# Kernel optimization log

Measured on AMD Instinct MI355X. Metric: run time of the kernel, lower is better.

## Reference

```python
import jax, jax.numpy as jnp
import numpy as np

N = 50000      # nodes
E = 250000     # edges
IN = 256       # in_channels
OUT = 256      # out_channels
H = 4          # heads
C = OUT // H   # per-head channels = 64
MSG = 128
TIME = 64
ED = MSG + TIME + 2   # edge_dim = 194


def _glorot(k, shape):
    return (jax.random.normal(k, shape, jnp.float32) / np.sqrt(shape[0])).astype(jnp.float32)


def setup_inputs() -> dict:
    ks = jax.random.split(jax.random.key(0), 16)
    z = lambda: jnp.zeros((H * C,), jnp.float32)
    inp = {
        "x": jax.random.normal(ks[0], (N, IN), jnp.float32),
        "edge_index": jax.random.randint(ks[1], (2, E), 0, N),
        "edge_attr": jax.random.normal(ks[2], (E, ED), jnp.float32),
        # conv1 params (in_channels=IN)
        "Wq1": _glorot(ks[3], (IN, H * C)), "bq1": z(),
        "Wk1": _glorot(ks[4], (IN, H * C)), "bk1": z(),
        "Wv1": _glorot(ks[5], (IN, H * C)), "bv1": z(),
        "We1": _glorot(ks[6], (ED, H * C)),              # lin_edge has no bias in PyG
        "Ws1": _glorot(ks[7], (IN, H * C)), "bs1": z(),  # skip/root connection
        # conv2 params (in_channels=OUT)
        "Wq2": _glorot(ks[8], (OUT, H * C)), "bq2": z(),
        "Wk2": _glorot(ks[9], (OUT, H * C)), "bk2": z(),
        "Wv2": _glorot(ks[10], (OUT, H * C)), "bv2": z(),
        "We2": _glorot(ks[11], (ED, H * C)),
        "Ws2": _glorot(ks[12], (OUT, H * C)), "bs2": z(),
    }
    return inp


def _tconv(x, src, dst, edge_attr, Wq, bq, Wk, bk, Wv, bv, We, Ws, bs):
    """PyG TransformerConv (heads=H, concat=True, root_weight=True), eval mode."""
    n = x.shape[0]
    q = (x @ Wq + bq).reshape(n, H, C)
    k = (x @ Wk + bk).reshape(n, H, C)
    v = (x @ Wv + bv).reshape(n, H, C)
    e = (edge_attr @ We).reshape(-1, H, C)          # [E,H,C]
    kj = k[src] + e                                  # key + edge embedding
    vj = v[src] + e                                  # value + edge embedding
    logits = jnp.einsum('ehc,ehc->eh', q[dst], kj) / np.sqrt(C)  # [E,H]
    # segment softmax over incoming edges of each dst node
    m = jax.lax.stop_gradient(jax.ops.segment_max(logits, dst, num_segments=n))
    ex = jnp.exp(logits - m[dst])
    denom = jax.ops.segment_sum(ex, dst, num_segments=n)
    a = ex / (denom[dst] + 1e-16)                    # [E,H]
    agg = jax.ops.segment_sum(vj * a[:, :, None], dst, num_segments=n)  # [N,H,C]
    return agg.reshape(n, H * C) + x @ Ws + bs


def reference(x, edge_index, edge_attr,
              Wq1, bq1, Wk1, bk1, Wv1, bv1, We1, Ws1, bs1,
              Wq2, bq2, Wk2, bk2, Wv2, bv2, We2, Ws2, bs2):
    src, dst = edge_index[0], edge_index[1]
    h = jax.nn.relu(_tconv(x, src, dst, edge_attr,
                           Wq1, bq1, Wk1, bk1, Wv1, bv1, We1, Ws1, bs1))
    # dropout is identity in eval mode
    return _tconv(h, src, dst, edge_attr,
                  Wq2, bq2, Wk2, bk2, Wv2, bv2, We2, Ws2, bs2)
```

## Files before the change

### kernel.cpp

```cpp
#include <hip/hip_runtime.h>

#define N_NODES 50000
#define N_EDGES 250000
#define DIM 256
#define ED 194
#define EDP 224
#define MP_NODE 50048
#define MP_EDGE 250112

typedef __bf16 bf16x8 __attribute__((ext_vector_type(8)));
typedef float f32x4 __attribute__((ext_vector_type(4)));
typedef short s16x8 __attribute__((ext_vector_type(8)));
typedef short s16x4 __attribute__((ext_vector_type(4)));
typedef unsigned short u16x8 __attribute__((ext_vector_type(8)));

__device__ __forceinline__ float bf2f(unsigned short b){
  union { unsigned int u; float f; } v; v.u = ((unsigned int)b)<<16; return v.f;
}
__device__ __forceinline__ short f2bf(float f){
  union { float f; unsigned int u; } v; v.f = f;
  unsigned int u = v.u;
  return (short)((u + 0x7fffu + ((u>>16)&1u))>>16);
}

__device__ __forceinline__ void gload_lds16(const void* g, void* l){
  __builtin_amdgcn_global_load_lds(
      (const __attribute__((address_space(1))) unsigned int*)g,
      (__attribute__((address_space(3))) unsigned int*)l, 16, 0, 0);
}

__global__ __launch_bounds__(256) void convert_x_kernel(
    const float* __restrict__ x, short* __restrict__ xb, int* __restrict__ deg)
{
  int idx = blockIdx.x*256 + threadIdx.x;
  if (idx < N_NODES) deg[idx] = 0;
  s16x4 o;
  if (idx < N_NODES*64){
    float4 a = *(const float4*)(x + (size_t)idx*4);
    o[0]=f2bf(a.x); o[1]=f2bf(a.y); o[2]=f2bf(a.z); o[3]=f2bf(a.w);
  } else {
    o[0]=0; o[1]=0; o[2]=0; o[3]=0;
  }
  *(s16x4*)(xb + (size_t)idx*4) = o;
}

#define E_ROWS 32
__global__ __launch_bounds__(256) void convert_e_kernel(
    const float* __restrict__ ea, short* __restrict__ eb)
{
  __shared__ float lds[E_ROWS*ED];
  int row0 = blockIdx.x * E_ROWS;
  int tid = threadIdx.x;
  int base = row0 * ED;
  int valid = N_EDGES*ED - base;

  for (int i = tid; i < E_ROWS*ED/4; i += 256){
    float4 v;
    if (i*4 < valid) v = *(const float4*)(ea + base + i*4);
    else             v = make_float4(0.f,0.f,0.f,0.f);
    *(float4*)(lds + i*4) = v;
  }
  __syncthreads();

  for (int u = tid; u < E_ROWS*28; u += 256){
    int row = u / 28;
    int c8  = u - row*28;
    int col = c8*8;
    s16x8 o;
    if (col + 8 <= ED){
      #pragma unroll
      for (int j2=0;j2<4;j2++){
        float2 f = *(const float2*)(lds + row*ED + col + j2*2);
        o[j2*2]   = f2bf(f.x);
        o[j2*2+1] = f2bf(f.y);
      }
    } else {
      #pragma unroll
      for (int j=0;j<8;j++){
        int c = col + j;
        o[j] = (c < ED) ? f2bf(lds[row*ED + c]) : (short)0;
      }
    }
    *(s16x8*)(eb + (size_t)(row0+row)*EDP + col) = o;
  }
}

__global__ __launch_bounds__(256) void prep_weights_all(
    const float* __restrict__ Wq1, const float* __restrict__ Wk1,
    const float* __restrict__ Wv1, const float* __restrict__ Ws1,
    const float* __restrict__ We1,
    const float* __restrict__ bq1, const float* __restrict__ bk1,
    const float* __restrict__ bv1, const float* __restrict__ bs1,
    const float* __restrict__ Wq2, const float* __restrict__ Wk2,
    const float* __restrict__ Wv2, const float* __restrict__ Ws2,
    const float* __restrict__ We2,
    const float* __restrict__ bq2, const float* __restrict__ bk2,
    const float* __restrict__ bv2, const float* __restrict__ bs2,
    short* __restrict__ WtN1, short* __restrict__ WtN2,
    short* __restrict__ WtE, float* __restrict__ biasN1, float* __restrict__ biasN2)
{
  __shared__ short lds[64*65];
  int b = blockIdx.x, tid = threadIdx.x;
  if (b < 128){
    int conv = b>>6, bb = b&63;
    int mat = bb>>4, tile = bb&15;
    int i0 = (tile>>2)*64, o0 = (tile&3)*64;
    const float* W = conv ? ((mat==0)?Wq2:((mat==1)?Wk2:((mat==2)?Wv2:Ws2)))
                          : ((mat==0)?Wq1:((mat==1)?Wk1:((mat==2)?Wv1:Ws1)));
    short* WtN = conv ? WtN2 : WtN1;
    #pragma unroll
    for (int t=0;t<16;t++){
      int idx = t*256+tid; int r = idx>>6, c = idx&63;
      lds[r*65+c] = f2bf(W[(size_t)(i0+r)*256 + o0 + c]);
    }
    __syncthreads();
    #pragma unroll
    for (int t=0;t<4;t++){
      int idx = t*256+tid; int r = idx>>4, c4 = (idx&15)*4;
      s16x4 o;
      o[0]=lds[(c4+0)*65+r]; o[1]=lds[(c4+1)*65+r];
      o[2]=lds[(c4+2)*65+r]; o[3]=lds[(c4+3)*65+r];
      *(s16x4*)(WtN + (mat<<16) + (o0+r)*256 + i0 + c4) = o;
    }
  } else if (b < 160){
    int b2 = b-128;
    int k0 = (b2>>3)*64, o0 = (b2&7)*64;
    const float* We = (o0 < 256) ? We1 : We2;
    int oc = o0 & 255;
    #pragma unroll
    for (int t=0;t<16;t++){
      int idx = t*256+tid; int r = idx>>6, c = idx&63;
      int k = k0+r;
      lds[r*65+c] = (k<ED) ? f2bf(We[(size_t)k*256 + oc + c]) : (short)0;
    }
    __syncthreads();
    #pragma unroll
    for (int t=0;t<4;t++){
      int idx = t*256+tid; int r = idx>>4, c4 = (idx&15)*4;
      if (k0 + c4 < EDP){
        s16x4 o;
        o[0]=lds[(c4+0)*65+r]; o[1]=lds[(c4+1)*65+r];
        o[2]=lds[(c4+2)*65+r]; o[3]=lds[(c4+3)*65+r];
        *(s16x4*)(WtE + (size_t)(o0+r)*EDP + k0 + c4) = o;
      }
    }
  } else {
    int conv = b - 160;
    float* biasN = conv ? biasN2 : biasN1;
    for (int t = tid; t < 1024; t += 256){
      const float* bb = conv ? ((t<256)?bq2:((t<512)?bk2:((t<768)?bv2:bs2)))
                             : ((t<256)?bq1:((t<512)?bk1:((t<768)?bv1:bs1)));
      biasN[t] = bb[t&255];
    }
  }
}

__global__ __launch_bounds__(256) void count_deg(const int* __restrict__ dst, int* __restrict__ deg){
  int e = blockIdx.x*256 + threadIdx.x;
  if (e < N_EDGES) atomicAdd(&deg[dst[e]], 1);
}
#define SCAN_NBLK 196
__global__ __launch_bounds__(256) void scan_p1(const int* __restrict__ deg, int* __restrict__ part){
  int t = threadIdx.x;
  int i = blockIdx.x*256 + t;
  int v = (i<N_NODES)? deg[i] : 0;
  #pragma unroll
  for (int off=32; off; off>>=1) v += __shfl_xor(v, off, 64);
  __shared__ int s[4];
  if ((t&63)==0) s[t>>6] = v;
  __syncthreads();
  if (t==0) part[blockIdx.x] = s[0]+s[1]+s[2]+s[3];
}
__global__ __launch_bounds__(256) void scan_p2(int* __restrict__ part){
  __shared__ int s[256];
  int t = threadIdx.x;
  int v = (t<SCAN_NBLK)? part[t] : 0;
  s[t] = v; __syncthreads();
  for (int off=1; off<256; off<<=1){
    int x = (t>=off)? s[t-off] : 0;
    __syncthreads();
    s[t] += x;
    __syncthreads();
  }
  part[t] = (t==0)? 0 : s[t-1];
}
__global__ __launch_bounds__(256) void scan_p3(const int* __restrict__ deg,
    const int* __restrict__ part, int* __restrict__ rowptr, int* __restrict__ cursor){
  __shared__ int s[256];
  int t = threadIdx.x;
  int i = blockIdx.x*256 + t;
  int v = (i<N_NODES)? deg[i] : 0;
  s[t] = v; __syncthreads();
  for (int off=1; off<256; off<<=1){
    int x = (t>=off)? s[t-off] : 0;
    __syncthreads();
    s[t] += x;
    __syncthreads();
  }
  if (i < N_NODES){ rowptr[i+1] = part[blockIdx.x] + s[t]; cursor[i] = 0; }
  if (i == 0) rowptr[0] = 0;
}
__global__ __launch_bounds__(256) void scatter_edges(
    const int* __restrict__ src, const int* __restrict__ dst,
    const int* __restrict__ rowptr, int* __restrict__ cursor, int2* __restrict__ csr)
{
  int e = blockIdx.x*256 + threadIdx.x;
  if (e < N_EDGES){
    int d = dst[e];
    int pos = atomicAdd(&cursor[d], 1);
    csr[rowptr[d] + pos] = make_int2(src[e]<<11, e<<10);
  }
}

template<int K, int NLD, bool HAS_BIAS, int SWZ_NB>
__global__ __launch_bounds__(256) void gemm_bt(
    const short* __restrict__ A, const short* __restrict__ Bt,
    const float* __restrict__ bias, short* __restrict__ out, int M)
{
  __shared__ short As[128*32];
  __shared__ short Bs[128*32];
  int tid = threadIdx.x;
  int lane = tid & 63, wave = tid >> 6;

  int mblk, nblk;
  if (SWZ_NB > 0){
    int bid = blockIdx.x;
    int MB  = gridDim.x / SWZ_NB;
    int MB8 = MB & ~7;
    int body = MB8 * SWZ_NB;
    if (bid < body){
      int xcd = bid & 7, w = bid >> 3;
      nblk = w % SWZ_NB;
      mblk = (w / SWZ_NB) * 8 + xcd;
    } else {
      int r = bid - body;
      mblk = MB8 + r / SWZ_NB;
      nblk = r % SWZ_NB;
    }
  } else {
    mblk = blockIdx.x; nblk = blockIdx.y;
  }
  int m0 = mblk*128, n0 = nblk*128;

  int srow = tid>>2, scol = (tid&3)*8;
  const short* gA = A + (size_t)(m0+srow)*K + scol;
  const short* gB = Bt + (size_t)(n0+srow)*K + scol;
  short* ldsA1 = As + wave*512;
  short* ldsA2 = As + 2048 + wave*512;
  short* ldsB1 = Bs + wave*512;
  short* ldsB2 = Bs + 2048 + wave*512;

  int wr = wave>>1, wc = wave&1;
  int fr = lane & 15;
  int kq = lane >> 4;
  f32x4 acc[4][4];
  #pragma unroll
  for (int a=0;a<4;a++)
    #pragma unroll
    for (int b=0;b<4;b++) acc[a][b] = (f32x4){0.f,0.f,0.f,0.f};

  for (int k0=0; k0<K; k0+=32){
    __syncthreads();
    gload_lds16(gA + k0,                ldsA1);
    gload_lds16(gA + (size_t)64*K + k0, ldsA2);
    gload_lds16(gB + k0,                ldsB1);
    gload_lds16(gB + (size_t)64*K + k0, ldsB2);
    __syncthreads();

    bf16x8 af[4], bf[4];
    const short* ar = As + (wr*64 + fr)*32 + kq*8;
    const short* br = Bs + (wc*64 + fr)*32 + kq*8;
    #pragma unroll
    for (int fm=0;fm<4;fm++) af[fm] = *(const bf16x8*)(ar + fm*512);
    #pragma unroll
    for (int fn=0;fn<4;fn++) bf[fn] = *(const bf16x8*)(br + fn*512);
    #pragma unroll
    for (int fm=0;fm<4;fm++)
      #pragma unroll
      for (int fn=0;fn<4;fn++)
        acc[fm][fn] = __builtin_amdgcn_mfma_f32_16x16x32_bf16(af[fm], bf[fn], acc[fm][fn], 0, 0, 0);
  }

  int cr = (lane>>4)*4;
  int cc = lane & 15;
  #pragma unroll
  for (int fm=0;fm<4;fm++){
    #pragma unroll
    for (int fn=0;fn<4;fn++){
      int col = n0 + wc*64 + fn*16 + cc;
      float bv = HAS_BIAS ? bias[col] : 0.f;
      #pragma unroll
      for (int i=0;i<4;i++){
        int row = m0 + wr*64 + fm*16 + cr + i;
        if (row < M) out[(size_t)row*NLD + col] = f2bf(acc[fm][fn][i] + bv);
      }
    }
  }
}

__global__ __launch_bounds__(256) void edge_phase_kernel(
    const short* __restrict__ QKVS, const short* __restrict__ Eemb,
    const int* __restrict__ rowptr, const int2* __restrict__ csr,
    short* __restrict__ out_bf, float* __restrict__ out_f, int relu)
{
  int tid = threadIdx.x, wave = tid>>6, lane = tid&63;
  int node = blockIdx.x*4 + wave;
  if (node >= N_NODES){
    if (node < MP_NODE && out_bf){
      s16x4 z; z[0]=0; z[1]=0; z[2]=0; z[3]=0;
      *(s16x4*)(out_bf + (size_t)node*256 + lane*4) = z;
    }
    return;
  }
  int half = lane>>5;
  int hl   = lane&31;
  int c8   = hl*8;
  const unsigned short* base = (const unsigned short*)QKVS + (size_t)node*1024;

  u16x8 qu = *(const u16x8*)(base + c8);
  float q[8];
  #pragma unroll
  for (int j=0;j<8;j++) q[j] = bf2f(qu[j])*0.125f;

  int beg = rowptr[node], end = rowptr[node+1];
  float l = 0.f;
  float a[8];
  #pragma unroll
  for (int j=0;j<8;j++) a[j] = 0.f;
  int kb = 512 + hl*16;
  int ebo = hl*16;

  if (beg < end){
    int j0 = beg + half;
    int2 se = csr[(j0 < end) ? j0 : (end-1)];
    for (int idx = beg; idx < end; idx += 2){
      int jn = idx + 2 + half;
      int2 se_n = csr[(jn < end) ? jn : (end-1)];
      int j = idx + half;
      const char* Kp = (const char*)QKVS + (unsigned)(se.x + kb);
      const char* Ep = (const char*)Eemb + (unsigned)(se.y + ebo);
      u16x8 ku = *(const u16x8*)Kp;
      u16x8 vu = *(const u16x8*)(Kp + 512);
      u16x8 eu = *(const u16x8*)Ep;
      float vv[8];
      float t = 0.f;
      #pragma unroll
      for (int c=0;c<8;c++){
        float ef = bf2f(eu[c]);
        float kf = bf2f(ku[c]) + ef;
        vv[c]    = bf2f(vu[c]) + ef;
        t += q[c]*kf;
      }
      t += __shfl_xor(t, 1, 64);
      t += __shfl_xor(t, 2, 64);
      t += __shfl_xor(t, 4, 64);
      float p = (j < end) ? __expf(t) : 0.f;
      l += p;
      #pragma unroll
      for (int c=0;c<8;c++) a[c] += p*vv[c];
      se = se_n;
    }
  }

  l += __shfl_xor(l, 32, 64);
  #pragma unroll
  for (int c=0;c<8;c++) a[c] += __shfl_xor(a[c], 32, 64);

  float inv = (l > 0.f) ? 1.0f/l : 0.f;
  u16x8 su = *(const u16x8*)(base + 768 + c8);
  float r[8];
  #pragma unroll
  for (int c=0;c<8;c++){
    float v = a[c]*inv + bf2f(su[c]);
    r[c] = relu ? fmaxf(v, 0.f) : v;
  }

  if (out_bf){
    if (!half){
      s16x8 o;
      #pragma unroll
      for (int c=0;c<8;c++) o[c] = f2bf(r[c]);
      *(s16x8*)(out_bf + (size_t)node*256 + c8) = o;
    }
  } else {
    float4 st = half ? make_float4(r[4],r[5],r[6],r[7])
                     : make_float4(r[0],r[1],r[2],r[3]);
    *(float4*)(out_f + (size_t)node*256 + c8 + half*4) = st;
  }
}

extern "C" void kernel_launch(void* const* d_in, const int* in_sizes, int n_in,
                              void* d_out, int out_size, void* d_ws, size_t ws_size,
                              hipStream_t stream)
{
  const float* x     = (const float*)d_in[0];
  const int*   eidx  = (const int*)d_in[1];
  const float* eattr = (const float*)d_in[2];
  const float* Wq1=(const float*)d_in[3],  *bq1=(const float*)d_in[4];
  const float* Wk1=(const float*)d_in[5],  *bk1=(const float*)d_in[6];
  const float* Wv1=(const float*)d_in[7],  *bv1=(const float*)d_in[8];
  const float* We1=(const float*)d_in[9];
  const float* Ws1=(const float*)d_in[10], *bs1=(const float*)d_in[11];
  const float* Wq2=(const float*)d_in[12], *bq2=(const float*)d_in[13];
  const float* Wk2=(const float*)d_in[14], *bk2=(const float*)d_in[15];
  const float* Wv2=(const float*)d_in[16], *bv2=(const float*)d_in[17];
  const float* We2=(const float*)d_in[18];
  const float* Ws2=(const float*)d_in[19], *bs2=(const float*)d_in[20];

  char* ws = (char*)d_ws;
  size_t off = 0;
  auto alloc = [&](size_t bytes)->char*{
    char* p = ws + off; off = (off + bytes + 255) & ~(size_t)255; return p;
  };
  short* QKVS  = (short*)alloc((size_t)N_NODES*1024*2);
  short* Eemb  = (short*)alloc((size_t)MP_EDGE*512*2);
  short* x_bf  = (short*)alloc((size_t)MP_NODE*DIM*2);
  short* h_bf  = (short*)alloc((size_t)MP_NODE*DIM*2);
  short* e_bf  = (short*)alloc((size_t)MP_EDGE*EDP*2);
  short* WtN1  = (short*)alloc((size_t)4*65536*2);
  short* WtN2  = (short*)alloc((size_t)4*65536*2);
  short* WtE   = (short*)alloc((size_t)512*EDP*2);
  float* biasN1= (float*)alloc((size_t)1024*4);
  float* biasN2= (float*)alloc((size_t)1024*4);
  int*   deg   = (int*)alloc((size_t)N_NODES*4);
  int*   rowptr= (int*)alloc((size_t)(N_NODES+1)*4);
  int*   cursor= (int*)alloc((size_t)N_NODES*4);
  int*   part  = (int*)alloc((size_t)256*4);
  int2*  csr   = (int2*)alloc((size_t)N_EDGES*8);

  const int* srcp = eidx;
  const int* dstp = eidx + N_EDGES;

  const int EB = (N_EDGES + 255)/256;

  convert_x_kernel<<<MP_NODE*64/256,256,0,stream>>>(x, x_bf, deg);
  convert_e_kernel<<<MP_EDGE/E_ROWS,256,0,stream>>>(eattr, e_bf);

  count_deg<<<EB,256,0,stream>>>(dstp, deg);
  scan_p1<<<SCAN_NBLK,256,0,stream>>>(deg, part);
  scan_p2<<<1,256,0,stream>>>(part);
  scan_p3<<<SCAN_NBLK,256,0,stream>>>(deg, part, rowptr, cursor);
  scatter_edges<<<EB,256,0,stream>>>(srcp, dstp, rowptr, cursor, csr);

  prep_weights_all<<<162,256,0,stream>>>(
      Wq1,Wk1,Wv1,Ws1,We1,bq1,bk1,bv1,bs1,
      Wq2,Wk2,Wv2,Ws2,We2,bq2,bk2,bv2,bs2,
      WtN1,WtN2,WtE,biasN1,biasN2);

  gemm_bt<EDP,512,false,4><<<(MP_EDGE/128)*4,256,0,stream>>>(e_bf, WtE, nullptr, Eemb, N_EDGES);

  gemm_bt<DIM,1024,true,0><<<dim3(MP_NODE/128,8),256,0,stream>>>(x_bf, WtN1, biasN1, QKVS, N_NODES);
  edge_phase_kernel<<<MP_NODE/4,256,0,stream>>>(QKVS,Eemb,rowptr,csr,h_bf,nullptr,1);

  gemm_bt<DIM,1024,true,0><<<dim3(MP_NODE/128,8),256,0,stream>>>(h_bf, WtN2, biasN2, QKVS, N_NODES);
  edge_phase_kernel<<<N_NODES/4,256,0,stream>>>(QKVS,Eemb+256,rowptr,csr,nullptr,(float*)d_out,0);
}
```

Measured before the change: 846.6 us.

## Double GEMM K-tile to 64 with XOR-swizzled LDS layout

```diff
diff --git a/kernel.cpp b/kernel.cpp
--- a/kernel.cpp
+++ b/kernel.cpp
@@ -4,7 +4,7 @@
 #define N_EDGES 250000
 #define DIM 256
 #define ED 194
-#define EDP 224
+#define EDP 256
 #define MP_NODE 50048
 #define MP_EDGE 250112
 
@@ -62,9 +62,9 @@
   }
   __syncthreads();
 
-  for (int u = tid; u < E_ROWS*28; u += 256){
-    int row = u / 28;
-    int c8  = u - row*28;
+  for (int u = tid; u < E_ROWS*32; u += 256){
+    int row = u >> 5;
+    int c8  = u & 31;
     int col = c8*8;
     s16x8 o;
     if (col + 8 <= ED){
@@ -217,8 +217,8 @@
     const short* __restrict__ A, const short* __restrict__ Bt,
     const float* __restrict__ bias, short* __restrict__ out, int M)
 {
-  __shared__ short As[128*32];
-  __shared__ short Bs[128*32];
+  __shared__ short As[128*64];
+  __shared__ short Bs[128*64];
   int tid = threadIdx.x;
   int lane = tid & 63, wave = tid >> 6;
 
@@ -242,43 +242,49 @@
   }
   int m0 = mblk*128, n0 = nblk*128;
 
-  int srow = tid>>2, scol = (tid&3)*8;
-  const short* gA = A + (size_t)(m0+srow)*K + scol;
-  const short* gB = Bt + (size_t)(n0+srow)*K + scol;
-  short* ldsA1 = As + wave*512;
-  short* ldsA2 = As + 2048 + wave*512;
-  short* ldsB1 = Bs + wave*512;
-  short* ldsB2 = Bs + 2048 + wave*512;
+  int srow = wave*8 + (lane>>3);
+  int sx   = ((lane&7) ^ ((lane>>3)&7))*8;
+  const short* gA = A + (size_t)(m0+srow)*K + sx;
+  const short* gB = Bt + (size_t)(n0+srow)*K + sx;
+  short* ldsA = As + wave*512;
+  short* ldsB = Bs + wave*512;
 
   int wr = wave>>1, wc = wave&1;
   int fr = lane & 15;
   int kq = lane >> 4;
+  int frx = fr & 7;
+  const short* arb = As + (wr*64 + fr)*64;
+  const short* brb = Bs + (wc*64 + fr)*64;
+
   f32x4 acc[4][4];
   #pragma unroll
   for (int a=0;a<4;a++)
     #pragma unroll
     for (int b=0;b<4;b++) acc[a][b] = (f32x4){0.f,0.f,0.f,0.f};
 
-  for (int k0=0; k0<K; k0+=32){
-    __syncthreads();
-    gload_lds16(gA + k0,                ldsA1);
-    gload_lds16(gA + (size_t)64*K + k0, ldsA2);
-    gload_lds16(gB + k0,                ldsB1);
-    gload_lds16(gB + (size_t)64*K + k0, ldsB2);
-    __syncthreads();
-
-    bf16x8 af[4], bf[4];
-    const short* ar = As + (wr*64 + fr)*32 + kq*8;
-    const short* br = Bs + (wc*64 + fr)*32 + kq*8;
-    #pragma unroll
-    for (int fm=0;fm<4;fm++) af[fm] = *(const bf16x8*)(ar + fm*512);
-    #pragma unroll
-    for (int fn=0;fn<4;fn++) bf[fn] = *(const bf16x8*)(br + fn*512);
-    #pragma unroll
-    for (int fm=0;fm<4;fm++)
-      #pragma unroll
-      for (int fn=0;fn<4;fn++)
-        acc[fm][fn] = __builtin_amdgcn_mfma_f32_16x16x32_bf16(af[fm], bf[fn], acc[fm][fn], 0, 0, 0);
+  for (int k0=0; k0<K; k0+=64){
+    __syncthreads();
+    #pragma unroll
+    for (int i=0;i<4;i++){
+      gload_lds16(gA + (size_t)i*32*K + k0, ldsA + i*2048);
+      gload_lds16(gB + (size_t)i*32*K + k0, ldsB + i*2048);
+    }
+    __syncthreads();
+
+    #pragma unroll
+    for (int ks=0; ks<2; ks++){
+      int cA = ((ks*4 + kq) ^ frx)*8;
+      bf16x8 af[4], bf[4];
+      #pragma unroll
+      for (int fm=0;fm<4;fm++) af[fm] = *(const bf16x8*)(arb + fm*1024 + cA);
+      #pragma unroll
+      for (int fn=0;fn<4;fn++) bf[fn] = *(const bf16x8*)(brb + fn*1024 + cA);
+      #pragma unroll
+      for (int fm=0;fm<4;fm++)
+        #pragma unroll
+        for (int fn=0;fn<4;fn++)
+          acc[fm][fn] = __builtin_amdgcn_mfma_f32_16x16x32_bf16(af[fm], bf[fn], acc[fm][fn], 0, 0, 0);
+    }
   }
 
   int cr = (lane>>4)*4;
```

New measurement: 820.9 us. -3.0%, faster.
